# Optimization experiments

Measured on AMD Instinct MI355X. Metric: run time of the kernel, lower is better.

The kernel has to match this reference:

```python
import jax, jax.numpy as jnp
import numpy as np

B, S, E, H = 2, 4096, 512, 8
DK = E // H


def setup_inputs() -> dict:
    k = jax.random.key(0)
    ks = jax.random.split(k, 11)
    sc = 0.02
    return {
        "query": jax.random.normal(ks[0], (B, S, E), jnp.float32),
        "key_in": jax.random.normal(ks[1], (B, S, E), jnp.float32),
        "value": jax.random.normal(ks[2], (B, S, E), jnp.float32),
        "Wq": jax.random.normal(ks[3], (E, E), jnp.float32) * sc,
        "bq": jax.random.normal(ks[4], (E,), jnp.float32) * sc,
        "Wk": jax.random.normal(ks[5], (E, E), jnp.float32) * sc,
        "bk": jax.random.normal(ks[6], (E,), jnp.float32) * sc,
        "Wv": jax.random.normal(ks[7], (E, E), jnp.float32) * sc,
        "bv": jax.random.normal(ks[8], (E,), jnp.float32) * sc,
        "Wo": jax.random.normal(ks[9], (E, E), jnp.float32) * sc,
        "bo": jax.random.normal(ks[10], (E,), jnp.float32) * sc,
    }


def reference(query, key_in, value, Wq, bq, Wk, bk, Wv, bv, Wo, bo):
    b, s, _ = query.shape
    # Linear projections
    q = query @ Wq + bq
    k = key_in @ Wk + bk
    v = value @ Wv + bv
    # [b, s, H, dk] -> [b, H, s, dk]
    q = q.reshape(b, s, H, DK).transpose(0, 2, 1, 3)
    k = k.reshape(b, s, H, DK).transpose(0, 2, 1, 3)
    v = v.reshape(b, s, H, DK).transpose(0, 2, 1, 3)
    # NOTE: source bug — softmax over UNSCALED scores (1/sqrt scaling in the
    # original is applied to a dead variable after softmax). Reproduce faithfully.
    scores = jnp.einsum("bhqd,bhkd->bhqk", q, k)  # [b,H,s,s] — O(N^2) materialized
    weights = jax.nn.softmax(scores.astype(jnp.float32), axis=-1)
    attn = jnp.einsum("bhqk,bhkd->bhqd", weights, v)
    # [b,H,s,dk] -> [b,s,E]
    concat = attn.transpose(0, 2, 1, 3).reshape(b, s, E)
    return concat @ Wo + bo
```

## Files before the change

### kernel.cpp

```cpp
#include <hip/hip_runtime.h>
#include <hip/hip_bf16.h>

#define B_  2
#define S_  4096
#define E_  512
#define H_  8
#define DK_ 64
#define M_  8192

typedef float f32x4  __attribute__((ext_vector_type(4)));
typedef float f32x16 __attribute__((ext_vector_type(16)));
typedef short s16x8  __attribute__((ext_vector_type(8)));
typedef short s16x4  __attribute__((ext_vector_type(4)));

static __device__ __forceinline__ short f2bf(float x) {
  __hip_bfloat16 h = __float2bfloat16(x);
  return __builtin_bit_cast(short, h);
}

static __device__ __forceinline__ f32x4 mfma32(s16x8 a, s16x8 b, f32x4 c) {
  return __builtin_amdgcn_mfma_f32_16x16x32_bf16(a, b, c, 0, 0, 0);
}

static __device__ __forceinline__ f32x16 mfma3232(s16x8 a, s16x8 b, f32x16 c) {
  return __builtin_amdgcn_mfma_f32_32x32x16_bf16(a, b, c, 0, 0, 0);
}

static __device__ __forceinline__ float fastexp2(float x) {
#if __has_builtin(__builtin_amdgcn_exp2f)
  return __builtin_amdgcn_exp2f(x);
#else
  return __expf(x * 0.69314718056f);
#endif
}

static __device__ __forceinline__ void gload_lds16(const void* g, void* l) {
  __builtin_amdgcn_global_load_lds(
      (const __attribute__((address_space(1))) unsigned int*)g,
      (__attribute__((address_space(3))) unsigned int*)l, 16, 0, 0);
}

__global__ __launch_bounds__(256) void conv_wT_all(
    const float* __restrict__ Wq, const float* __restrict__ Wk,
    const float* __restrict__ Wv, const float* __restrict__ Wo,
    short* __restrict__ Wt) {
  const float* W = (blockIdx.y == 0) ? Wq
                   : ((blockIdx.y == 1) ? Wk : ((blockIdx.y == 2) ? Wv : Wo));
  short* o = Wt + (size_t)blockIdx.y * (E_ * E_);
  int idx = blockIdx.x * 256 + threadIdx.x;
  int j = idx >> 9, k = idx & 511;
  o[idx] = f2bf(W[(size_t)k * E_ + j]);
}

static __device__ __forceinline__ void gemm_core_512(
    const short* __restrict__ A, const short* __restrict__ Bt,
    short* As, short* Bs, int tm, int tn, f32x4 acc[4][4]) {
  const int tid = threadIdx.x;
  const int wave = tid >> 6, lane = tid & 63;
  const int c = lane & 15, g = lane >> 4;
  int fOff[2];
#pragma unroll
  for (int r = 0; r < 2; ++r) {
    const int f = wave * 2 + r;
    fOff[r] = ((f >> 2) * 64 + (f & 3) * 16 + c) * 512 + g * 8;
  }
  auto stg = [&](int p, int b) {
#pragma unroll
    for (int r = 0; r < 2; ++r) {
      const int f = wave * 2 + r;
      gload_lds16(A + (size_t)tm * 512 + p * 32 + fOff[r],
                  (char*)As + b * 8192 + f * 1024);
      gload_lds16(Bt + (size_t)tn * 512 + p * 32 + fOff[r],
                  (char*)Bs + b * 8192 + f * 1024);
    }
  };
  stg(0, 0);
  __syncthreads();
  for (int p = 0; p < 16; ++p) {
    if (p + 1 < 16) stg(p + 1, (p + 1) & 1);
    const short* Ac = As + (p & 1) * 4096;
    const short* Bc = Bs + (p & 1) * 4096;
    s16x8 af[4], bfr[4];
#pragma unroll
    for (int i = 0; i < 4; ++i)
      af[i] = *(const s16x8*)(Ac + ((wave >> 1) * 4 + i) * 512 + lane * 8);
#pragma unroll
    for (int j = 0; j < 4; ++j)
      bfr[j] = *(const s16x8*)(Bc + ((wave & 1) * 4 + j) * 512 + lane * 8);
#pragma unroll
    for (int i = 0; i < 4; ++i)
#pragma unroll
      for (int j = 0; j < 4; ++j)
        acc[i][j] = mfma32(af[i], bfr[j], acc[i][j]);
    __syncthreads();
  }
}

static __device__ __forceinline__ void gemm_core_f32A(
    const float* __restrict__ A, const short* __restrict__ Bt,
    short* As, short* Bs, int tm, int tn, f32x4 acc[4][4]) {
  const int tid = threadIdx.x;
  const int wave = tid >> 6, lane = tid & 63;
  const int c = lane & 15, g = lane >> 4;
  int fOff[2];
#pragma unroll
  for (int r = 0; r < 2; ++r) {
    const int f = wave * 2 + r;
    fOff[r] = ((f >> 2) * 64 + (f & 3) * 16 + c) * 512 + g * 8;
  }
  auto stgB = [&](int p, int b) {
#pragma unroll
    for (int r = 0; r < 2; ++r)
      gload_lds16(Bt + (size_t)tn * 512 + p * 32 + fOff[r],
                  (char*)Bs + b * 8192 + (wave * 2 + r) * 1024);
  };
  float4 a0[2], a1[2];
  auto ldA = [&](int p) {
#pragma unroll
    for (int r = 0; r < 2; ++r) {
      const float* ap = A + (size_t)tm * 512 + p * 32 + fOff[r];
      a0[r] = *(const float4*)ap;
      a1[r] = *(const float4*)(ap + 4);
    }
  };
  auto wrA = [&](int b) {
#pragma unroll
    for (int r = 0; r < 2; ++r) {
      s16x8 w;
      w[0] = f2bf(a0[r].x); w[1] = f2bf(a0[r].y);
      w[2] = f2bf(a0[r].z); w[3] = f2bf(a0[r].w);
      w[4] = f2bf(a1[r].x); w[5] = f2bf(a1[r].y);
      w[6] = f2bf(a1[r].z); w[7] = f2bf(a1[r].w);
      *(s16x8*)((char*)As + b * 8192 + (wave * 2 + r) * 1024 + lane * 16) = w;
    }
  };
  ldA(0); stgB(0, 0); wrA(0);
  __syncthreads();
  for (int p = 0; p < 16; ++p) {
    if (p + 1 < 16) { ldA(p + 1); stgB(p + 1, (p + 1) & 1); }
    const short* Ac = As + (p & 1) * 4096;
    const short* Bc = Bs + (p & 1) * 4096;
    s16x8 af[4], bfr[4];
#pragma unroll
    for (int i = 0; i < 4; ++i)
      af[i] = *(const s16x8*)(Ac + ((wave >> 1) * 4 + i) * 512 + lane * 8);
#pragma unroll
    for (int j = 0; j < 4; ++j)
      bfr[j] = *(const s16x8*)(Bc + ((wave & 1) * 4 + j) * 512 + lane * 8);
#pragma unroll
    for (int i = 0; i < 4; ++i)
#pragma unroll
      for (int j = 0; j < 4; ++j)
        acc[i][j] = mfma32(af[i], bfr[j], acc[i][j]);
    if (p + 1 < 16) wrA((p + 1) & 1);
    __syncthreads();
  }
}

__global__ __launch_bounds__(256) void gemm_qkv(
    const float* __restrict__ Xq, const float* __restrict__ Xk,
    const float* __restrict__ Xv, const short* __restrict__ Wt,
    const float* __restrict__ bq, const float* __restrict__ bk,
    const float* __restrict__ bv,
    short* __restrict__ Qo, short* __restrict__ Ko, short* __restrict__ Vto) {
  __shared__ __align__(16) short As[2 * 4096];
  __shared__ __align__(16) short Bs[2 * 4096];
  const int z = blockIdx.z;
  const float* A = (z == 0) ? Xq : ((z == 1) ? Xk : Xv);
  const short* Bt = Wt + z * (E_ * E_);
  const float* bias = (z == 0) ? bq : ((z == 1) ? bk : bv);
  const int tm = blockIdx.x * 128, tn = blockIdx.y * 128;
  f32x4 acc[4][4] = {};
  gemm_core_f32A(A, Bt, As, Bs, tm, tn, acc);

  const int tid = threadIdx.x;
  const int wave = tid >> 6, lane = tid & 63;
  const int wm = (wave >> 1) * 64, wn = (wave & 1) * 64;
  const int c = lane & 15, g = lane >> 4;
#pragma unroll
  for (int i = 0; i < 4; ++i) {
#pragma unroll
    for (int j = 0; j < 4; ++j) {
      const int gc = tn + wn + j * 16 + c;
      const float bb = bias[gc];
      const int h = gc >> 6, dk = gc & 63;
      if (z == 2) {
        const int gr0 = tm + wm + i * 16 + g * 4;
        const int b = gr0 >> 12, s0 = gr0 & 4095;
        s16x4 v4;
#pragma unroll
        for (int r = 0; r < 4; ++r) v4[r] = f2bf(acc[i][j][r] + bb);
        *(s16x4*)&Vto[(size_t)((b * H_ + h) * DK_ + dk) * S_ + s0] = v4;
      } else {
#pragma unroll
        for (int r = 0; r < 4; ++r) {
          const int gr = tm + wm + i * 16 + g * 4 + r;
          const int b = gr >> 12, s = gr & 4095;
          float v = acc[i][j][r] + bb;
          if (z == 0) v *= 1.44269504f;
          const short hv = f2bf(v);
          if (z == 1)
            Ko[(size_t)((b * H_ + h) * S_ + s) * DK_ + dk] = hv;
          else
            Qo[(size_t)((b * H_ + h) * S_ + s) * DK_ + dk] = hv;
        }
      }
    }
  }
}

__global__ __launch_bounds__(256) void gemm_out(
    const short* __restrict__ AO, const short* __restrict__ Wot,
    const float* __restrict__ bo, float* __restrict__ out) {
  __shared__ __align__(16) short As[2 * 4096];
  __shared__ __align__(16) short Bs[2 * 4096];
  const int tm = blockIdx.x * 128, tn = blockIdx.y * 128;
  f32x4 acc[4][4] = {};
  gemm_core_512(AO, Wot, As, Bs, tm, tn, acc);

  const int tid = threadIdx.x;
  const int wave = tid >> 6, lane = tid & 63;
  const int wm = (wave >> 1) * 64, wn = (wave & 1) * 64;
  const int c = lane & 15, g = lane >> 4;
#pragma unroll
  for (int i = 0; i < 4; ++i) {
#pragma unroll
    for (int j = 0; j < 4; ++j) {
      const int gc = tn + wn + j * 16 + c;
      const float bb = bo[gc];
#pragma unroll
      for (int r = 0; r < 4; ++r) {
        const int gr = tm + wm + i * 16 + g * 4 + r;
        out[(size_t)gr * E_ + gc] = acc[i][j][r] + bb;
      }
    }
  }
}

__global__ __launch_bounds__(256, 2) void attn_fwd(
    const short* __restrict__ Q, const short* __restrict__ K,
    const short* __restrict__ Vt, short* __restrict__ O) {
  __shared__ __align__(16) char lds[49152];
  const int tid = threadIdx.x;
  const int wave = tid >> 6, lane = tid & 63;
  const int g = wave >> 1, kh = wave & 1;
  const int qi = lane & 31, hi = lane >> 5;
  const int bh = blockIdx.y;
  const int b = bh >> 3, h = bh & 7;
  const int q0 = blockIdx.x * 128 + g * 64;
  const short* Qp = Q + (size_t)bh * S_ * DK_;
  const short* Kp = K + (size_t)bh * S_ * DK_;
  const short* Vp = Vt + (size_t)bh * DK_ * S_;

  s16x8 qfL[4], qfH[4];
#pragma unroll
  for (int s = 0; s < 4; ++s) {
    qfL[s] = *(const s16x8*)(Qp + (size_t)(q0 + qi) * DK_ + s * 16 + hi * 8);
    qfH[s] = *(const s16x8*)(Qp + (size_t)(q0 + 32 + qi) * DK_ + s * 16 + hi * 8);
  }

  f32x16 o00 = {}, o01 = {}, o10 = {}, o11 = {};
  float lsL = 0.f, lsH = 0.f;

  int kOffL[2], vOffL[2];
#pragma unroll
  for (int r = 0; r < 2; ++r) {
    const int f = wave * 2 + r;
    const int row = (f >> 2) * 32 + qi;
    const int srow = (row & 32) | ((row & 8) << 1) | ((row & 4) << 1) |
                     ((row & 16) >> 2) | (row & 3);
    kOffL[r] = srow * DK_ + (f & 3) * 16 + hi * 8;
    vOffL[r] = ((f >> 2) * 32 + qi) * S_ + ((f >> 1) & 1) * 32 +
               (f & 1) * 16 + hi * 8;
  }

  auto stage = [&](int kt) {
#pragma unroll
    for (int r = 0; r < 2; ++r) {
      const int f = wave * 2 + r;
      gload_lds16(Kp + (size_t)kt * 64 * DK_ + kOffL[r],
                  lds + (kt % 3) * 8192 + f * 1024);
      gload_lds16(Vp + (size_t)kt * 64 + vOffL[r],
                  lds + 24576 + (kt % 3) * 8192 + f * 1024);
    }
  };

  auto bar4 = [&]() {
    asm volatile("s_waitcnt vmcnt(4) lgkmcnt(0)" ::: "memory");
    __builtin_amdgcn_s_barrier();
  };
  auto bar0 = [&]() {
    asm volatile("s_waitcnt vmcnt(0) lgkmcnt(0)" ::: "memory");
    __builtin_amdgcn_s_barrier();
  };

  const int lbK = kh * 4096 + (lane << 4);

  auto qk = [&](int t, f32x16& sL, f32x16& sH) {
    const char* Kc = lds + (t % 3) * 8192 + lbK;
    f32x16 a = {}, c = {};
    __builtin_amdgcn_s_setprio(1);
#pragma unroll
    for (int s = 0; s < 4; ++s) {
      s16x8 ka = *(const s16x8*)(Kc + s * 1024);
      a = mfma3232(ka, qfL[s], a);
      c = mfma3232(ka, qfH[s], c);
    }
    __builtin_amdgcn_s_setprio(0);
    sL = a; sH = c;
  };

  auto softpv = [&](const f32x16& sL, const f32x16& sH, int t) {
    const char* Vc = lds + 24576 + (t % 3) * 8192 + kh * 2048 + (lane << 4);
    float pL[16], pH[16];
#pragma unroll
    for (int r = 0; r < 16; ++r) { pL[r] = fastexp2(sL[r]); pH[r] = fastexp2(sH[r]); }
    float aL = 0.f, aH = 0.f;
#pragma unroll
    for (int r = 0; r < 16; ++r) { aL += pL[r]; aH += pH[r]; }
    lsL += aL; lsH += aH;
    s16x8 pbL[2], pbH[2];
#pragma unroll
    for (int ks = 0; ks < 2; ++ks)
#pragma unroll
      for (int j = 0; j < 8; ++j) {
        const int r = (j & 3) | (ks << 2) | ((j >> 2) << 3);
        pbL[ks][j] = f2bf(pL[r]);
        pbH[ks][j] = f2bf(pH[r]);
      }
    __builtin_amdgcn_s_setprio(1);
#pragma unroll
    for (int ks = 0; ks < 2; ++ks) {
      s16x8 va0 = *(const s16x8*)(Vc + ks * 1024);
      s16x8 va1 = *(const s16x8*)(Vc + 4096 + ks * 1024);
      o00 = mfma3232(va0, pbL[ks], o00);
      o01 = mfma3232(va0, pbH[ks], o01);
      o10 = mfma3232(va1, pbL[ks], o10);
      o11 = mfma3232(va1, pbH[ks], o11);
    }
    __builtin_amdgcn_s_setprio(0);
  };

  const int NT = S_ / 64;
  f32x16 sA0, sA1, sB0, sB1;

  stage(0);
  stage(1);
  bar4();
  qk(0, sA0, sA1);

  for (int t = 0; t < NT; t += 2) {
    if (t + 2 < NT) { stage(t + 2); bar4(); } else { bar0(); }
    qk(t + 1, sB0, sB1);
    softpv(sA0, sA1, t);
    if (t + 3 < NT) { stage(t + 3); bar4(); } else { bar0(); }
    if (t + 2 < NT) qk(t + 2, sA0, sA1);
    softpv(sB0, sB1, t + 1);
  }

  lsL += __shfl_xor(lsL, 32);
  lsH += __shfl_xor(lsH, 32);

  float* mrg = (float*)lds;
  const int mi = (g * 64 + lane) * 36;
  __syncthreads();
  if (kh) {
#pragma unroll
    for (int r = 0; r < 4; ++r) {
      *(f32x4*)(mrg + mi + r * 4) =
          f32x4{o00[r * 4], o00[r * 4 + 1], o00[r * 4 + 2], o00[r * 4 + 3]};
      *(f32x4*)(mrg + mi + 16 + r * 4) =
          f32x4{o01[r * 4], o01[r * 4 + 1], o01[r * 4 + 2], o01[r * 4 + 3]};
    }
    mrg[mi + 32] = lsL;
    mrg[mi + 33] = lsH;
  }
  __syncthreads();
  float rlL = 0.f, rlH = 0.f;
  if (!kh) {
#pragma unroll
    for (int r = 0; r < 16; ++r) {
      o00[r] += mrg[mi + r];
      o01[r] += mrg[mi + 16 + r];
    }
    rlL = 1.f / (lsL + mrg[mi + 32]);
    rlH = 1.f / (lsH + mrg[mi + 33]);
  }
  __syncthreads();
  if (kh) {
#pragma unroll
    for (int r = 0; r < 4; ++r) {
      *(f32x4*)(mrg + mi + r * 4) =
          f32x4{o10[r * 4], o10[r * 4 + 1], o10[r * 4 + 2], o10[r * 4 + 3]};
      *(f32x4*)(mrg + mi + 16 + r * 4) =
          f32x4{o11[r * 4], o11[r * 4 + 1], o11[r * 4 + 2], o11[r * 4 + 3]};
    }
  }
  __syncthreads();
  if (!kh) {
#pragma unroll
    for (int r = 0; r < 16; ++r) {
      o10[r] += mrg[mi + r];
      o11[r] += mrg[mi + 16 + r];
    }
    short* OpL = O + ((size_t)(b * S_ + q0 + qi)) * E_ + h * DK_;
    short* OpH = O + ((size_t)(b * S_ + q0 + 32 + qi)) * E_ + h * DK_;
#pragma unroll
    for (int rr = 0; rr < 4; ++rr) {
      s16x4 vL0, vL1, vH0, vH1;
#pragma unroll
      for (int e = 0; e < 4; ++e) {
        vL0[e] = f2bf(o00[rr * 4 + e] * rlL);
        vL1[e] = f2bf(o10[rr * 4 + e] * rlL);
        vH0[e] = f2bf(o01[rr * 4 + e] * rlH);
        vH1[e] = f2bf(o11[rr * 4 + e] * rlH);
      }
      *(s16x4*)(OpL + rr * 8 + hi * 4) = vL0;
      *(s16x4*)(OpL + 32 + rr * 8 + hi * 4) = vL1;
      *(s16x4*)(OpH + rr * 8 + hi * 4) = vH0;
      *(s16x4*)(OpH + 32 + rr * 8 + hi * 4) = vH1;
    }
  }
}

extern "C" void kernel_launch(void* const* d_in, const int* in_sizes, int n_in,
                              void* d_out, int out_size, void* d_ws, size_t ws_size,
                              hipStream_t stream) {
  const float* query  = (const float*)d_in[0];
  const float* key_in = (const float*)d_in[1];
  const float* value  = (const float*)d_in[2];
  const float* Wq = (const float*)d_in[3];
  const float* bq = (const float*)d_in[4];
  const float* Wk = (const float*)d_in[5];
  const float* bk = (const float*)d_in[6];
  const float* Wv = (const float*)d_in[7];
  const float* bv = (const float*)d_in[8];
  const float* Wo = (const float*)d_in[9];
  const float* bo = (const float*)d_in[10];
  float* out = (float*)d_out;

  const size_t NA = (size_t)M_ * E_;
  short* ws  = (short*)d_ws;
  short* Wt  = ws;
  short* Wot = Wt + 3 * E_ * E_;
  short* Qb  = Wt + 4 * E_ * E_;
  short* Kb  = Qb + NA;
  short* Vtb = Kb + NA;
  short* AO  = Vtb + NA;

  conv_wT_all<<<dim3(E_ * E_ / 256, 4), 256, 0, stream>>>(Wq, Wk, Wv, Wo, Wt);

  gemm_qkv<<<dim3(M_ / 128, E_ / 128, 3), 256, 0, stream>>>(
      query, key_in, value, Wt, bq, bk, bv, Qb, Kb, Vtb);
  attn_fwd<<<dim3(S_ / 128, B_ * H_), 256, 0, stream>>>(Qb, Kb, Vtb, AO);
  gemm_out<<<dim3(M_ / 128, E_ / 128), 256, 0, stream>>>(AO, Wot, bo, out);
}
```

Before: 148.2 us.

## Widen attention blocks to 256 queries with a six-stage shared K/V ring

```diff
diff --git a/kernel.cpp b/kernel.cpp
--- a/kernel.cpp
+++ b/kernel.cpp
@@ -237,17 +237,17 @@
   }
 }
 
-__global__ __launch_bounds__(256, 2) void attn_fwd(
+__global__ __launch_bounds__(512, 2) void attn_fwd(
     const short* __restrict__ Q, const short* __restrict__ K,
     const short* __restrict__ Vt, short* __restrict__ O) {
-  __shared__ __align__(16) char lds[49152];
+  __shared__ __align__(16) char lds[98304];
   const int tid = threadIdx.x;
   const int wave = tid >> 6, lane = tid & 63;
   const int g = wave >> 1, kh = wave & 1;
   const int qi = lane & 31, hi = lane >> 5;
   const int bh = blockIdx.y;
   const int b = bh >> 3, h = bh & 7;
-  const int q0 = blockIdx.x * 128 + g * 64;
+  const int q0 = blockIdx.x * 256 + g * 64;
   const short* Qp = Q + (size_t)bh * S_ * DK_;
   const short* Kp = K + (size_t)bh * S_ * DK_;
   const short* Vp = Vt + (size_t)bh * DK_ * S_;
@@ -262,27 +262,22 @@
   f32x16 o00 = {}, o01 = {}, o10 = {}, o11 = {};
   float lsL = 0.f, lsH = 0.f;
 
-  int kOffL[2], vOffL[2];
-#pragma unroll
-  for (int r = 0; r < 2; ++r) {
-    const int f = wave * 2 + r;
-    const int row = (f >> 2) * 32 + qi;
+  int kOff, vOff;
+  {
+    const int j = wave;
+    const int row = (j >> 2) * 32 + qi;
     const int srow = (row & 32) | ((row & 8) << 1) | ((row & 4) << 1) |
                      ((row & 16) >> 2) | (row & 3);
-    kOffL[r] = srow * DK_ + (f & 3) * 16 + hi * 8;
-    vOffL[r] = ((f >> 2) * 32 + qi) * S_ + ((f >> 1) & 1) * 32 +
-               (f & 1) * 16 + hi * 8;
+    kOff = srow * DK_ + (j & 3) * 16 + hi * 8;
+    vOff = ((j >> 2) * 32 + qi) * S_ + ((j >> 1) & 1) * 32 +
+           (j & 1) * 16 + hi * 8;
   }
 
   auto stage = [&](int kt) {
-#pragma unroll
-    for (int r = 0; r < 2; ++r) {
-      const int f = wave * 2 + r;
-      gload_lds16(Kp + (size_t)kt * 64 * DK_ + kOffL[r],
-                  lds + (kt % 3) * 8192 + f * 1024);
-      gload_lds16(Vp + (size_t)kt * 64 + vOffL[r],
-                  lds + 24576 + (kt % 3) * 8192 + f * 1024);
-    }
+    gload_lds16(Kp + (size_t)kt * 64 * DK_ + kOff,
+                lds + (kt % 6) * 8192 + wave * 1024);
+    gload_lds16(Vp + (size_t)kt * 64 + vOff,
+                lds + 49152 + (kt % 6) * 8192 + wave * 1024);
   };
 
   auto bar4 = [&]() {
@@ -297,7 +292,7 @@
   const int lbK = kh * 4096 + (lane << 4);
 
   auto qk = [&](int t, f32x16& sL, f32x16& sH) {
-    const char* Kc = lds + (t % 3) * 8192 + lbK;
+    const char* Kc = lds + (t % 6) * 8192 + lbK;
     f32x16 a = {}, c = {};
     __builtin_amdgcn_s_setprio(1);
 #pragma unroll
@@ -311,7 +306,7 @@
   };
 
   auto softpv = [&](const f32x16& sL, const f32x16& sH, int t) {
-    const char* Vc = lds + 24576 + (t % 3) * 8192 + kh * 2048 + (lane << 4);
+    const char* Vc = lds + 49152 + (t % 6) * 8192 + kh * 2048 + (lane << 4);
     float pL[16], pH[16];
 #pragma unroll
     for (int r = 0; r < 16; ++r) { pL[r] = fastexp2(sL[r]); pH[r] = fastexp2(sH[r]); }
@@ -344,17 +339,14 @@
   const int NT = S_ / 64;
   f32x16 sA0, sA1, sB0, sB1;
 
-  stage(0);
-  stage(1);
+  stage(0); stage(1); stage(2); stage(3);
   bar4();
-  qk(0, sA0, sA1);
 
   for (int t = 0; t < NT; t += 2) {
-    if (t + 2 < NT) { stage(t + 2); bar4(); } else { bar0(); }
+    if (t + 4 < NT) { stage(t + 4); stage(t + 5); bar4(); } else bar0();
+    qk(t, sA0, sA1);
     qk(t + 1, sB0, sB1);
     softpv(sA0, sA1, t);
-    if (t + 3 < NT) { stage(t + 3); bar4(); } else { bar0(); }
-    if (t + 2 < NT) qk(t + 2, sA0, sA1);
     softpv(sB0, sB1, t + 1);
   }
 
@@ -452,6 +444,6 @@
 
   gemm_qkv<<<dim3(M_ / 128, E_ / 128, 3), 256, 0, stream>>>(
       query, key_in, value, Wt, bq, bk, bv, Qb, Kb, Vtb);
-  attn_fwd<<<dim3(S_ / 128, B_ * H_), 256, 0, stream>>>(Qb, Kb, Vtb, AO);
+  attn_fwd<<<dim3(S_ / 256, B_ * H_), 512, 0, stream>>>(Qb, Kb, Vtb, AO);
   gemm_out<<<dim3(M_ / 128, E_ / 128), 256, 0, stream>>>(AO, Wot, bo, out);
 }
```

Measured after the change: 144.7 us. 2.4% less time.
